# Performance work log

Hardware: AMD Instinct MI355X
Metric: run time of the kernel (lower is better)

Reference implementation:

```python
import jax, jax.numpy as jnp
import numpy as np
import math

IN_SRC, IN_DST, OUT, H = 64, 64, 128, 8
DK = OUT // H


def setup_inputs() -> dict:
    key = jax.random.key(0)
    ks = jax.random.split(key, 24)
    f = lambda k, shp, s=0.05: (jax.random.normal(k, shp, dtype=jnp.float32) * s)
    B, n, m = 16, 256, 128
    inp = {
        'h_dst': jax.random.normal(ks[0], (B, n, IN_DST), dtype=jnp.float32),
        'h_src': jax.random.normal(ks[1], (B, m, IN_SRC), dtype=jnp.float32),
        'h_edge': jax.random.normal(ks[2], (B, n, m), dtype=jnp.float32),
        'ope_ma_adj': jax.random.randint(ks[3], (B, n, m), 0, 2, dtype=jnp.int32),
        'ope_oo_adj': jax.random.randint(ks[4], (B, n, n), 0, 2, dtype=jnp.int32),
        'batch_idxes': jnp.arange(B, dtype=jnp.int64),
        'Wq': f(ks[5], (OUT, IN_DST)), 'bq': f(ks[6], (OUT,)),
        'Wk': f(ks[7], (OUT, IN_SRC)), 'bk': f(ks[8], (OUT,)),
        'Wkd': f(ks[9], (OUT, IN_DST)), 'bkd': f(ks[10], (OUT,)),
        'Wke': f(ks[11], (OUT, 1)), 'bke': f(ks[12], (OUT,)),
        'Wv': f(ks[13], (OUT, IN_SRC)), 'bv': f(ks[14], (OUT,)),
        'Wvd': f(ks[15], (OUT, IN_DST)), 'bvd': f(ks[16], (OUT,)),
        'Wa': f(ks[17], (OUT, OUT)), 'ba': f(ks[18], (OUT,)),
        'rel_pri': jnp.ones((2, H), dtype=jnp.float32),
        'rel_att': f(ks[19], (2, H, DK, DK), 0.2),
        'rel_msg': f(ks[20], (2, H, DK, DK), 0.2),
        'skip': jnp.ones((1,), dtype=jnp.float32),
    }
    return inp


def reference(h_dst, h_src, h_edge, ope_ma_adj, ope_oo_adj, batch_idxes,
              Wq, bq, Wk, bk, Wkd, bkd, Wke, bke, Wv, bv, Wvd, bvd, Wa, ba,
              rel_pri, rel_att, rel_msg, skip):
    B = batch_idxes.shape[0]
    n, m = h_dst.shape[1], h_src.shape[1]
    adj_ma = ope_ma_adj[batch_idxes].astype(jnp.float32)  # [B,n,m]
    adj_oo = ope_oo_adj[batch_idxes].astype(jnp.float32)  # [B,n,n]
    inv_sqrt_dk = 1.0 / math.sqrt(DK)
    # torch einsum 'abcd,abdd->abcd' multiplies by the diagonal of the relation matrix
    dA0 = jnp.diagonal(rel_att[0], axis1=-2, axis2=-1)  # [H,DK]
    dA1 = jnp.diagonal(rel_att[1], axis1=-2, axis2=-1)
    dM0 = jnp.diagonal(rel_msg[0], axis1=-2, axis2=-1)
    dM1 = jnp.diagonal(rel_msg[1], axis1=-2, axis2=-1)

    q = (h_dst @ Wq.T + bq).reshape(B, n, H, DK)           # [B,n,H,DK]
    k = ((h_src @ Wk.T + bk).reshape(B, m, H, DK)) * dA0   # [B,m,H,DK]
    scale0 = rel_pri[0] * inv_sqrt_dk                      # [H]
    m_o_att = jnp.einsum('bnhd,bmhd->bnmh', q, k) * scale0

    # edge projection: Linear(1->OUT) on h_edge[...,None]
    edge = (h_edge[..., None] * Wke[:, 0] + bke).reshape(B, n, m, H, DK) * dA0
    ee = jnp.einsum('bnhd,bnmhd->bnmh', q, edge) * scale0
    m_att = jax.nn.leaky_relu(adj_ma[..., None] * m_o_att + ee, 0.1)

    kd = ((h_dst @ Wkd.T + bkd).reshape(B, n, H, DK)) * dA1
    scale1 = rel_pri[1] * inv_sqrt_dk
    o_att = jax.nn.leaky_relu(adj_oo[..., None] * jnp.einsum('bnhd,bmhd->bnmh', q, kd) * scale1, 0.1)

    att = jnp.concatenate([m_att, o_att], axis=2)          # [B,n,m+n,H]
    mask = jnp.concatenate([adj_ma, adj_oo], axis=2)[..., None] == 1
    att = jax.nn.softmax(jnp.where(mask, att, -1e9), axis=2)
    att_m, att_o = att[:, :, :m], att[:, :, m:]

    v = ((h_src @ Wv.T + bv).reshape(B, m, H, DK)) * dM0   # [B,m,H,DK]
    # m_res_msg = edge + v[:,None]; weighted sum over m (no [B,n,m,H,DK] extra alloc)
    a_m = (jnp.einsum('bnmh,bnmhd->bnhd', att_m, edge)
           + jnp.einsum('bnmh,bmhd->bnhd', att_m, v))
    c = ((h_dst @ Wvd.T + bvd).reshape(B, n, H, DK)) * dM1
    # o_res_msg[b,i,j] = c[b,i] + c[b,j]; weighted sum over j
    a_o = (jnp.einsum('bnjh,bjhd->bnhd', att_o, c)
           + att_o.sum(axis=2)[..., None] * c)

    res = (a_m + a_o).reshape(B, n, OUT)
    trans = jax.nn.gelu(res, approximate=False) @ Wa.T + ba
    alpha = jax.nn.sigmoid(skip[0])
    out = trans * alpha + q.reshape(B, n, OUT) * (1.0 - alpha)
    return out
```

## Files before the change

### kernel.cpp

```cpp
#include <hip/hip_runtime.h>
#include <math.h>

#define H 8
#define DK 16
#define OUTC 128
#define INC 64
#define NB 16
#define NN 256
#define NM 128

typedef float f32x4 __attribute__((ext_vector_type(4)));
typedef short s16x4 __attribute__((ext_vector_type(4)));
typedef short s16x8 __attribute__((ext_vector_type(8)));

#if __has_builtin(__builtin_amdgcn_mfma_f32_16x16x16bf16_1k)
__device__ __forceinline__ f32x4 MFMA16(s16x4 a, s16x4 b, f32x4 c) {
    return __builtin_amdgcn_mfma_f32_16x16x16bf16_1k(a, b, c, 0, 0, 0);
}
#else
__device__ __forceinline__ f32x4 MFMA16(s16x4 a, s16x4 b, f32x4 c) {
    s16x8 a8 = {a[0], a[1], a[2], a[3], 0, 0, 0, 0};
    s16x8 b8 = {b[0], b[1], b[2], b[3], 0, 0, 0, 0};
    return __builtin_amdgcn_mfma_f32_16x16x32_bf16(a8, b8, c, 0, 0, 0);
}
#endif

__device__ __forceinline__ unsigned short f2bf(float x) {
    unsigned int u = __float_as_uint(x);
    return (unsigned short)((u + 0x7fffu + ((u >> 16) & 1u)) >> 16);
}
__device__ __forceinline__ float bf2f(unsigned short s) {
    return __uint_as_float(((unsigned int)s) << 16);
}

__global__ __launch_bounds__(256) void proj_pack(
    const float* __restrict__ h_dst, const float* __restrict__ h_src,
    const int* __restrict__ adj_ma, const int* __restrict__ adj_oo,
    const float* __restrict__ Wq, const float* __restrict__ bq,
    const float* __restrict__ Wk, const float* __restrict__ bk,
    const float* __restrict__ Wkd, const float* __restrict__ bkd,
    const float* __restrict__ Wv, const float* __restrict__ bv,
    const float* __restrict__ Wvd, const float* __restrict__ bvd,
    const float* __restrict__ rel_pri, const float* __restrict__ rel_att,
    const float* __restrict__ rel_msg,
    float* __restrict__ qbuf, unsigned short* __restrict__ qpk,
    unsigned short* __restrict__ kpk, unsigned short* __restrict__ vcb,
    unsigned long long* __restrict__ mk)
{
    __shared__ float X_s[64 * 68];
    __shared__ float WT_s[64 * 128];

    int t = threadIdx.x;
    int bid = blockIdx.x;

    if (bid >= 256) {
        int w = ((bid - 256) << 2) + (t >> 6);
        int l = t & 63;
        #pragma unroll
        for (int i = 0; i < 16; ++i) {
            int flat = w * 16 + i;
            int row = flat / 6, g = flat - row * 6;
            int a = (g < 2) ? adj_ma[(long)row * NM + (g << 6) + l]
                            : adj_oo[(long)row * NN + ((g - 2) << 6) + l];
            unsigned long long m = __ballot(a != 0);
            if (l == 0) mk[flat] = m;
        }
        return;
    }

    int type, grow0;
    const float *X, *W, *bias;
    if (bid < 64)        { type = 0; grow0 = bid * 64;        X = h_dst; W = Wq;  bias = bq;  }
    else if (bid < 128)  { type = 2; grow0 = (bid-64) * 64;   X = h_dst; W = Wkd; bias = bkd; }
    else if (bid < 192)  { type = 4; grow0 = (bid-128) * 64;  X = h_dst; W = Wvd; bias = bvd; }
    else if (bid < 224)  { type = 1; grow0 = (bid-192) * 64;  X = h_src; W = Wk;  bias = bk;  }
    else                 { type = 3; grow0 = (bid-224) * 64;  X = h_src; W = Wv;  bias = bv;  }

    #pragma unroll
    for (int p = 0; p < 4; ++p) {
        int idx = t + 256 * p;
        int row = idx >> 4, part = idx & 15;
        float4 v = *(const float4*)(X + (long)(grow0 + row) * INC + part * 4);
        *(float4*)(X_s + row * 68 + part * 4) = v;
    }
    #pragma unroll
    for (int p = 0; p < 8; ++p) {
        int idx = t + 256 * p;
        int o = idx >> 4, part = idx & 15;
        float4 v = *(const float4*)(W + (long)o * INC + part * 4);
        int q0 = o >> 2, ob = o & 3;
        WT_s[(part*4+0)*128 + (((q0 ^ ((part*4+0)&31))<<2) + ob)] = v.x;
        WT_s[(part*4+1)*128 + (((q0 ^ ((part*4+1)&31))<<2) + ob)] = v.y;
        WT_s[(part*4+2)*128 + (((q0 ^ ((part*4+2)&31))<<2) + ob)] = v.z;
        WT_s[(part*4+3)*128 + (((q0 ^ ((part*4+3)&31))<<2) + ob)] = v.w;
    }
    __syncthreads();

    int o4 = t & 31;
    int rq = t >> 5;
    float4 acc[8];
    #pragma unroll
    for (int rr = 0; rr < 8; ++rr) acc[rr] = make_float4(0.f, 0.f, 0.f, 0.f);

    #pragma unroll 4
    for (int i4 = 0; i4 < 16; ++i4) {
        float4 w0 = *(const float4*)(WT_s + (i4*4+0)*128 + ((o4 ^ ((i4*4+0)&31))<<2));
        float4 w1 = *(const float4*)(WT_s + (i4*4+1)*128 + ((o4 ^ ((i4*4+1)&31))<<2));
        float4 w2 = *(const float4*)(WT_s + (i4*4+2)*128 + ((o4 ^ ((i4*4+2)&31))<<2));
        float4 w3 = *(const float4*)(WT_s + (i4*4+3)*128 + ((o4 ^ ((i4*4+3)&31))<<2));
        #pragma unroll
        for (int rr = 0; rr < 8; ++rr) {
            float4 x = *(const float4*)(X_s + (rq + 8*rr) * 68 + i4*4);
            acc[rr].x += x.x*w0.x + x.y*w1.x + x.z*w2.x + x.w*w3.x;
            acc[rr].y += x.x*w0.y + x.y*w1.y + x.z*w2.y + x.w*w3.y;
            acc[rr].z += x.x*w0.z + x.y*w1.z + x.z*w2.z + x.w*w3.z;
            acc[rr].w += x.x*w0.w + x.y*w1.w + x.z*w2.w + x.w*w3.w;
        }
    }

    int obase = o4 * 4;
    int head = o4 >> 2;
    float4 bs = *(const float4*)(bias + obase);
    float scl[4];
    #pragma unroll
    for (int c = 0; c < 4; ++c) {
        int o = obase + c;
        int hh = o >> 4, d = o & 15;
        float v = 1.f;
        if (type == 1)      v = rel_pri[hh]     * 0.25f * rel_att[(hh*DK + d)*DK + d];
        else if (type == 2) v = rel_pri[H + hh] * 0.25f * rel_att[((H + hh)*DK + d)*DK + d];
        else if (type == 3) v = rel_msg[(hh*DK + d)*DK + d];
        else if (type == 4) v = rel_msg[((H + hh)*DK + d)*DK + d];
        scl[c] = v;
    }
    #pragma unroll
    for (int rr = 0; rr < 8; ++rr) {
        int grow = grow0 + rq + 8*rr;
        float4 r4;
        r4.x = (acc[rr].x + bs.x) * scl[0];
        r4.y = (acc[rr].y + bs.y) * scl[1];
        r4.z = (acc[rr].z + bs.z) * scl[2];
        r4.w = (acc[rr].w + bs.w) * scl[3];
        unsigned int lo = (unsigned int)f2bf(r4.x) | ((unsigned int)f2bf(r4.y) << 16);
        unsigned int hi = (unsigned int)f2bf(r4.z) | ((unsigned int)f2bf(r4.w) << 16);
        uint2 pk = make_uint2(lo, hi);
        if (type == 0) {
            *(float4*)(qbuf + (long)grow * OUTC + obase) = r4;
            int b = grow >> 8, row = grow & 255;
            int lane = ((o4 & 3) << 4) + (row & 15);
            ((uint2*)qpk)[(long)((b*H + head)*16 + (row >> 4)) * 64 + lane] = pk;
        } else if (type == 1 || type == 2) {
            int b, key;
            if (type == 1) { b = grow >> 7; key = grow & 127; }
            else           { b = grow >> 8; key = 128 + (grow & 255); }
            int lane = (key & 15) + ((o4 & 3) << 4);
            ((uint2*)kpk)[(long)((b*H + head)*24 + (key >> 4)) * 64 + lane] = pk;
        } else {
            int b, key;
            if (type == 3) { b = grow >> 7; key = grow & 127; }
            else           { b = grow >> 8; key = 128 + (grow & 255); }
            ((uint2*)vcb)[(long)((b*H + head)*384 + key) * 4 + (o4 & 3)] = pk;
        }
    }
}

__global__ __launch_bounds__(256) void hgt_main5(
    const float* __restrict__ h_edge,
    const unsigned long long* __restrict__ mkbuf,
    const float* __restrict__ Wke, const float* __restrict__ bke,
    const float* __restrict__ rel_pri, const float* __restrict__ rel_att,
    const float* __restrict__ qbuf,
    const unsigned short* __restrict__ qpk,
    const unsigned short* __restrict__ kpk,
    const unsigned short* __restrict__ vcb,
    float* __restrict__ gelbuf)
{
    __shared__ unsigned short kpk_s[6144];
    __shared__ unsigned short vpk_s[6144];
    __shared__ float he_s[128 * 65];
    __shared__ unsigned long long mk_s[384];
    __shared__ float stats_s[256];
    __shared__ float s1s2_s[128];

    int t = threadIdx.x;
    int bid = blockIdx.x;
    int qb = bid & 3;
    int bh = bid >> 2;
    int h = bh & 7;
    int b = bh >> 3;
    int row0 = b * NN + qb * 64;

    {
        const uint4* src = (const uint4*)(kpk + (long)bh * 6144);
        uint4* dst = (uint4*)kpk_s;
        #pragma unroll
        for (int p = 0; p < 3; ++p) dst[t + 256*p] = src[t + 256*p];
    }
    #pragma unroll
    for (int p = 0; p < 6; ++p) {
        int idx = t + 256 * p;
        int key = idx >> 2, dc = idx & 3;
        uint2 v = ((const uint2*)(vcb + (long)bh * 6144))[key * 4 + dc];
        int base = (key >> 4) * 256 + ((((key >> 2) & 3) << 4) + dc * 4) * 4 + (key & 3);
        vpk_s[base     ] = (unsigned short)(v.x & 0xffffu);
        vpk_s[base + 4 ] = (unsigned short)(v.x >> 16);
        vpk_s[base + 8 ] = (unsigned short)(v.y & 0xffffu);
        vpk_s[base + 12] = (unsigned short)(v.y >> 16);
    }
    #pragma unroll
    for (int p = 0; p < 8; ++p) {
        int idx = t + 256 * p;
        int q = idx >> 5, jc = (idx & 31) << 2;
        float4 v = *(const float4*)(h_edge + (long)(row0 + q) * NM + jc);
        he_s[(jc+0)*65 + q] = v.x;
        he_s[(jc+1)*65 + q] = v.y;
        he_s[(jc+2)*65 + q] = v.z;
        he_s[(jc+3)*65 + q] = v.w;
    }
    for (int i = t; i < 384; i += 256) mk_s[i] = mkbuf[(long)row0 * 6 + i];
    if (t < 64) {
        const float* qr = qbuf + (long)(row0 + t) * OUTC + h * DK;
        float s1 = 0.f, s2 = 0.f;
        #pragma unroll
        for (int d = 0; d < DK; ++d) {
            int o = h * DK + d;
            float qq = qr[d] * rel_att[o * DK + d];
            s1 += qq * Wke[o];
            s2 += qq * bke[o];
        }
        float sc = rel_pri[h] * 0.25f;
        s1s2_s[t*2]   = s1 * sc;
        s1s2_s[t*2+1] = s2 * sc;
    }
    __syncthreads();

    int w = t >> 6, l = t & 63;
    int qi = l & 15;
    int grpb = (l >> 4) << 2;
    int qloc = w * 16 + qi;

    union { uint2 u; s16x4 s; } qf;
    qf.u = ((const uint2*)qpk)[(long)(bh * 16 + qb * 4 + w) * 64 + l];

    float S1q = s1s2_s[qloc * 2], S2q = s1s2_s[qloc * 2 + 1];
    unsigned int mdw[12];
    #pragma unroll
    for (int i = 0; i < 12; ++i) mdw[i] = ((const unsigned int*)(mk_s + qloc * 6))[i];

    float sum = 0.f, t0 = 0.f, t1 = 0.f, so = 0.f;
    f32x4 O0 = {0.f, 0.f, 0.f, 0.f};
    f32x4 O1 = {0.f, 0.f, 0.f, 0.f};
    const f32x4 zero = {0.f, 0.f, 0.f, 0.f};

    #pragma unroll
    for (int tt = 0; tt < 24; ++tt) {
        s16x4 kf = *(const s16x4*)(kpk_s + tt * 256 + l * 4);
        f32x4 s4 = MFMA16(kf, qf.s, zero);

        unsigned int dw = mdw[tt >> 1];
        int sb = ((tt & 1) << 4) + grpb;
        float ev[4], hev[4];
        #pragma unroll
        for (int r = 0; r < 4; ++r) {
            float x = s4[r];
            if (tt < 8) {
                hev[r] = he_s[(tt * 16 + grpb + r) * 65 + qloc];
                x += hev[r] * S1q + S2q;
            }
            float lk = fmaxf(x, 0.1f * x);
            float ex = __expf(lk);
            ev[r] = ((dw >> (sb + r)) & 1u) ? ex : 0.f;
        }
        float es = (ev[0] + ev[1]) + (ev[2] + ev[3]);
        sum += es;
        if (tt < 8) {
            t0 += es;
            t1 += (ev[0]*hev[0] + ev[1]*hev[1]) + (ev[2]*hev[2] + ev[3]*hev[3]);
        } else {
            so += es;
        }
        s16x4 p;
        p[0] = (short)f2bf(ev[0]); p[1] = (short)f2bf(ev[1]);
        p[2] = (short)f2bf(ev[2]); p[3] = (short)f2bf(ev[3]);
        s16x4 vf = *(const s16x4*)(vpk_s + tt * 256 + l * 4);
        if (tt & 1) O1 = MFMA16(p, vf, O1);
        else        O0 = MFMA16(p, vf, O0);
    }
    f32x4 O = O0 + O1;

    sum += __shfl_xor(sum, 16); sum += __shfl_xor(sum, 32);
    t0  += __shfl_xor(t0, 16);  t0  += __shfl_xor(t0, 32);
    t1  += __shfl_xor(t1, 16);  t1  += __shfl_xor(t1, 32);
    so  += __shfl_xor(so, 16);  so  += __shfl_xor(so, 32);
    if (l < 16) {
        float4 st = make_float4(1.f / sum, t0, t1, so);
        *(float4*)(stats_s + (w * 16 + l) * 4) = st;
    }

    int d = qi;
    int o = h * DK + d;
    float a0 = rel_att[o * DK + d];
    float wk = Wke[o], bk = bke[o];
    #pragma unroll
    for (int r = 0; r < 4; ++r) {
        int ql = w * 16 + grpb + r;
        float4 st = *(const float4*)(stats_s + ql * 4);
        int key = 128 + qb * 64 + ql;
        float cs = bf2f(vpk_s[(key >> 4) * 256 + ((((key >> 2) & 3) << 4) + d) * 4 + (key & 3)]);
        float res = st.x * (O[r] + a0 * (wk * st.z + bk * st.y) + st.w * cs);
        float g = 0.5f * res * (1.f + erff(res * 0.70710678118654752f));
        gelbuf[(long)(row0 + ql) * OUTC + o] = g;
    }
}

__global__ __launch_bounds__(256) void out_gemm(
    const float* __restrict__ gelbuf, const float* __restrict__ qbuf,
    const float* __restrict__ Wa, const float* __restrict__ ba,
    const float* __restrict__ skip, float* __restrict__ outp)
{
    __shared__ float WaT[128 * 128];
    __shared__ float gel_s[16 * 132];

    int t = threadIdx.x;
    long row0 = (long)blockIdx.x * 16;

    #pragma unroll
    for (int p = 0; p < 16; ++p) {
        int idx = t + 256 * p;
        int o = idx >> 5, part = idx & 31;
        float4 v = *(const float4*)(Wa + (long)o * OUTC + part * 4);
        int q0 = o >> 2, ob = o & 3;
        WaT[(part*4+0)*128 + (((q0 ^ ((part*4+0)&31))<<2) + ob)] = v.x;
        WaT[(part*4+1)*128 + (((q0 ^ ((part*4+1)&31))<<2) + ob)] = v.y;
        WaT[(part*4+2)*128 + (((q0 ^ ((part*4+2)&31))<<2) + ob)] = v.z;
        WaT[(part*4+3)*128 + (((q0 ^ ((part*4+3)&31))<<2) + ob)] = v.w;
    }
    #pragma unroll
    for (int p = 0; p < 2; ++p) {
        int idx = t + 256 * p;
        int row = idx >> 5, part = idx & 31;
        float4 v = *(const float4*)(gelbuf + (row0 + row) * OUTC + part * 4);
        *(float4*)(gel_s + row * 132 + part * 4) = v;
    }
    __syncthreads();

    int o4 = t & 31, rp = t >> 5;
    float4 acc0 = make_float4(0.f,0.f,0.f,0.f);
    float4 acc1 = make_float4(0.f,0.f,0.f,0.f);
    #pragma unroll 4
    for (int i4 = 0; i4 < 32; ++i4) {
        float4 w0 = *(const float4*)(WaT + (i4*4+0)*128 + ((o4 ^ ((i4*4+0)&31))<<2));
        float4 w1 = *(const float4*)(WaT + (i4*4+1)*128 + ((o4 ^ ((i4*4+1)&31))<<2));
        float4 w2 = *(const float4*)(WaT + (i4*4+2)*128 + ((o4 ^ ((i4*4+2)&31))<<2));
        float4 w3 = *(const float4*)(WaT + (i4*4+3)*128 + ((o4 ^ ((i4*4+3)&31))<<2));
        float4 x0 = *(const float4*)(gel_s + rp * 132 + i4*4);
        float4 x1 = *(const float4*)(gel_s + (rp+8) * 132 + i4*4);
        acc0.x += x0.x*w0.x + x0.y*w1.x + x0.z*w2.x + x0.w*w3.x;
        acc0.y += x0.x*w0.y + x0.y*w1.y + x0.z*w2.y + x0.w*w3.y;
        acc0.z += x0.x*w0.z + x0.y*w1.z + x0.z*w2.z + x0.w*w3.z;
        acc0.w += x0.x*w0.w + x0.y*w1.w + x0.z*w2.w + x0.w*w3.w;
        acc1.x += x1.x*w0.x + x1.y*w1.x + x1.z*w2.x + x1.w*w3.x;
        acc1.y += x1.x*w0.y + x1.y*w1.y + x1.z*w2.y + x1.w*w3.y;
        acc1.z += x1.x*w0.z + x1.y*w1.z + x1.z*w2.z + x1.w*w3.z;
        acc1.w += x1.x*w0.w + x1.y*w1.w + x1.z*w2.w + x1.w*w3.w;
    }

    float alpha = 1.f / (1.f + __expf(-skip[0]));
    float beta = 1.f - alpha;
    float4 bs = *(const float4*)(ba + o4*4);
    {
        float4 q0 = *(const float4*)(qbuf + (row0 + rp) * OUTC + o4*4);
        float4 r0;
        r0.x = alpha*(acc0.x + bs.x) + beta*q0.x;
        r0.y = alpha*(acc0.y + bs.y) + beta*q0.y;
        r0.z = alpha*(acc0.z + bs.z) + beta*q0.z;
        r0.w = alpha*(acc0.w + bs.w) + beta*q0.w;
        *(float4*)(outp + (row0 + rp) * OUTC + o4*4) = r0;
    }
    {
        float4 q1 = *(const float4*)(qbuf + (row0 + rp + 8) * OUTC + o4*4);
        float4 r1;
        r1.x = alpha*(acc1.x + bs.x) + beta*q1.x;
        r1.y = alpha*(acc1.y + bs.y) + beta*q1.y;
        r1.z = alpha*(acc1.z + bs.z) + beta*q1.z;
        r1.w = alpha*(acc1.w + bs.w) + beta*q1.w;
        *(float4*)(outp + (row0 + rp + 8) * OUTC + o4*4) = r1;
    }
}

extern "C" void kernel_launch(void* const* d_in, const int* in_sizes, int n_in,
                              void* d_out, int out_size, void* d_ws, size_t ws_size,
                              hipStream_t stream) {
    const float* h_dst  = (const float*)d_in[0];
    const float* h_src  = (const float*)d_in[1];
    const float* h_edge = (const float*)d_in[2];
    const int*   adj_ma = (const int*)d_in[3];
    const int*   adj_oo = (const int*)d_in[4];
    const float* Wq  = (const float*)d_in[6];
    const float* bq  = (const float*)d_in[7];
    const float* Wk  = (const float*)d_in[8];
    const float* bk  = (const float*)d_in[9];
    const float* Wkd = (const float*)d_in[10];
    const float* bkd = (const float*)d_in[11];
    const float* Wke = (const float*)d_in[12];
    const float* bke = (const float*)d_in[13];
    const float* Wv  = (const float*)d_in[14];
    const float* bv  = (const float*)d_in[15];
    const float* Wvd = (const float*)d_in[16];
    const float* bvd = (const float*)d_in[17];
    const float* Wa  = (const float*)d_in[18];
    const float* ba  = (const float*)d_in[19];
    const float* rel_pri = (const float*)d_in[20];
    const float* rel_att = (const float*)d_in[21];
    const float* rel_msg = (const float*)d_in[22];
    const float* skip    = (const float*)d_in[23];

    char* ws = (char*)d_ws;
    float* qbuf   = (float*)ws;
    float* gelbuf = (float*)(ws + 2097152);
    unsigned short* kpk = (unsigned short*)(ws + 4194304);
    unsigned short* qpk = (unsigned short*)(ws + 5767168);
    unsigned short* vcb = (unsigned short*)(ws + 6815744);
    unsigned long long* mkbuf = (unsigned long long*)(ws + 8388608);

    proj_pack<<<640, 256, 0, stream>>>(h_dst, h_src, adj_ma, adj_oo,
                                       Wq, bq, Wk, bk, Wkd, bkd, Wv, bv, Wvd, bvd,
                                       rel_pri, rel_att, rel_msg,
                                       qbuf, qpk, kpk, vcb, mkbuf);

    hgt_main5<<<NB * H * 4, 256, 0, stream>>>(
        h_edge, mkbuf, Wke, bke, rel_pri, rel_att,
        qbuf, qpk, kpk, vcb, gelbuf);

    out_gemm<<<NB * NN / 16, 256, 0, stream>>>(gelbuf, qbuf, Wa, ba, skip, (float*)d_out);
}
```

Baseline: 39.16 us.

## Fuse three kernels into one cooperative persistent kernel with grid syncs

After: 127.6 us. +225.7%, slower.

```diff
diff --git a/kernel.cpp b/kernel.cpp
--- a/kernel.cpp
+++ b/kernel.cpp
@@ -1,5 +1,8 @@
 #include <hip/hip_runtime.h>
+#include <hip/hip_cooperative_groups.h>
 #include <math.h>
+
+namespace cg = cooperative_groups;
 
 #define H 8
 #define DK 16
@@ -33,48 +36,44 @@
     return __uint_as_float(((unsigned int)s) << 16);
 }
 
-__global__ __launch_bounds__(256) void proj_pack(
-    const float* __restrict__ h_dst, const float* __restrict__ h_src,
-    const int* __restrict__ adj_ma, const int* __restrict__ adj_oo,
-    const float* __restrict__ Wq, const float* __restrict__ bq,
-    const float* __restrict__ Wk, const float* __restrict__ bk,
-    const float* __restrict__ Wkd, const float* __restrict__ bkd,
-    const float* __restrict__ Wv, const float* __restrict__ bv,
-    const float* __restrict__ Wvd, const float* __restrict__ bvd,
-    const float* __restrict__ rel_pri, const float* __restrict__ rel_att,
-    const float* __restrict__ rel_msg,
-    float* __restrict__ qbuf, unsigned short* __restrict__ qpk,
-    unsigned short* __restrict__ kpk, unsigned short* __restrict__ vcb,
-    unsigned long long* __restrict__ mk)
-{
-    __shared__ float X_s[64 * 68];
-    __shared__ float WT_s[64 * 128];
-
-    int t = threadIdx.x;
-    int bid = blockIdx.x;
-
-    if (bid >= 256) {
-        int w = ((bid - 256) << 2) + (t >> 6);
+struct KArgs {
+    const float* h_dst; const float* h_src; const float* h_edge;
+    const int* adj_ma; const int* adj_oo;
+    const float* Wq; const float* bq; const float* Wk; const float* bk;
+    const float* Wkd; const float* bkd; const float* Wke; const float* bke;
+    const float* Wv; const float* bv; const float* Wvd; const float* bvd;
+    const float* Wa; const float* ba;
+    const float* rel_pri; const float* rel_att; const float* rel_msg;
+    const float* skip;
+    float* qbuf; unsigned short* qpk; unsigned short* kpk; unsigned short* vcb;
+    unsigned long long* mk; float* gelbuf; float* outp;
+};
+
+__device__ __forceinline__ void proj_unit_body(const KArgs& A, int unit, int t,
+                                               float* X_s, float* WT_s)
+{
+    if (unit >= 256) {
+        int w = ((unit - 256) << 2) + (t >> 6);
         int l = t & 63;
         #pragma unroll
         for (int i = 0; i < 16; ++i) {
             int flat = w * 16 + i;
             int row = flat / 6, g = flat - row * 6;
-            int a = (g < 2) ? adj_ma[(long)row * NM + (g << 6) + l]
-                            : adj_oo[(long)row * NN + ((g - 2) << 6) + l];
+            int a = (g < 2) ? A.adj_ma[(long)row * NM + (g << 6) + l]
+                            : A.adj_oo[(long)row * NN + ((g - 2) << 6) + l];
             unsigned long long m = __ballot(a != 0);
-            if (l == 0) mk[flat] = m;
+            if (l == 0) A.mk[flat] = m;
         }
         return;
     }
 
     int type, grow0;
     const float *X, *W, *bias;
-    if (bid < 64)        { type = 0; grow0 = bid * 64;        X = h_dst; W = Wq;  bias = bq;  }
-    else if (bid < 128)  { type = 2; grow0 = (bid-64) * 64;   X = h_dst; W = Wkd; bias = bkd; }
-    else if (bid < 192)  { type = 4; grow0 = (bid-128) * 64;  X = h_dst; W = Wvd; bias = bvd; }
-    else if (bid < 224)  { type = 1; grow0 = (bid-192) * 64;  X = h_src; W = Wk;  bias = bk;  }
-    else                 { type = 3; grow0 = (bid-224) * 64;  X = h_src; W = Wv;  bias = bv;  }
+    if (unit < 64)        { type = 0; grow0 = unit * 64;        X = A.h_dst; W = A.Wq;  bias = A.bq;  }
+    else if (unit < 128)  { type = 2; grow0 = (unit-64) * 64;   X = A.h_dst; W = A.Wkd; bias = A.bkd; }
+    else if (unit < 192)  { type = 4; grow0 = (unit-128) * 64;  X = A.h_dst; W = A.Wvd; bias = A.bvd; }
+    else if (unit < 224)  { type = 1; grow0 = (unit-192) * 64;  X = A.h_src; W = A.Wk;  bias = A.bk;  }
+    else                  { type = 3; grow0 = (unit-224) * 64;  X = A.h_src; W = A.Wv;  bias = A.bv;  }
 
     #pragma unroll
     for (int p = 0; p < 4; ++p) {
@@ -127,10 +126,10 @@
         int o = obase + c;
         int hh = o >> 4, d = o & 15;
         float v = 1.f;
-        if (type == 1)      v = rel_pri[hh]     * 0.25f * rel_att[(hh*DK + d)*DK + d];
-        else if (type == 2) v = rel_pri[H + hh] * 0.25f * rel_att[((H + hh)*DK + d)*DK + d];
-        else if (type == 3) v = rel_msg[(hh*DK + d)*DK + d];
-        else if (type == 4) v = rel_msg[((H + hh)*DK + d)*DK + d];
+        if (type == 1)      v = A.rel_pri[hh]     * 0.25f * A.rel_att[(hh*DK + d)*DK + d];
+        else if (type == 2) v = A.rel_pri[H + hh] * 0.25f * A.rel_att[((H + hh)*DK + d)*DK + d];
+        else if (type == 3) v = A.rel_msg[(hh*DK + d)*DK + d];
+        else if (type == 4) v = A.rel_msg[((H + hh)*DK + d)*DK + d];
         scl[c] = v;
     }
     #pragma unroll
@@ -145,53 +144,37 @@
         unsigned int hi = (unsigned int)f2bf(r4.z) | ((unsigned int)f2bf(r4.w) << 16);
         uint2 pk = make_uint2(lo, hi);
         if (type == 0) {
-            *(float4*)(qbuf + (long)grow * OUTC + obase) = r4;
+            *(float4*)(A.qbuf + (long)grow * OUTC + obase) = r4;
             int b = grow >> 8, row = grow & 255;
             int lane = ((o4 & 3) << 4) + (row & 15);
-            ((uint2*)qpk)[(long)((b*H + head)*16 + (row >> 4)) * 64 + lane] = pk;
+            ((uint2*)A.qpk)[(long)((b*H + head)*16 + (row >> 4)) * 64 + lane] = pk;
         } else if (type == 1 || type == 2) {
             int b, key;
             if (type == 1) { b = grow >> 7; key = grow & 127; }
             else           { b = grow >> 8; key = 128 + (grow & 255); }
             int lane = (key & 15) + ((o4 & 3) << 4);
-            ((uint2*)kpk)[(long)((b*H + head)*24 + (key >> 4)) * 64 + lane] = pk;
+            ((uint2*)A.kpk)[(long)((b*H + head)*24 + (key >> 4)) * 64 + lane] = pk;
         } else {
             int b, key;
             if (type == 3) { b = grow >> 7; key = grow & 127; }
             else           { b = grow >> 8; key = 128 + (grow & 255); }
-            ((uint2*)vcb)[(long)((b*H + head)*384 + key) * 4 + (o4 & 3)] = pk;
-        }
-    }
-}
-
-__global__ __launch_bounds__(256) void hgt_main5(
-    const float* __restrict__ h_edge,
-    const unsigned long long* __restrict__ mkbuf,
-    const float* __restrict__ Wke, const float* __restrict__ bke,
-    const float* __restrict__ rel_pri, const float* __restrict__ rel_att,
-    const float* __restrict__ qbuf,
-    const unsigned short* __restrict__ qpk,
-    const unsigned short* __restrict__ kpk,
-    const unsigned short* __restrict__ vcb,
-    float* __restrict__ gelbuf)
-{
-    __shared__ unsigned short kpk_s[6144];
-    __shared__ unsigned short vpk_s[6144];
-    __shared__ float he_s[128 * 65];
-    __shared__ unsigned long long mk_s[384];
-    __shared__ float stats_s[256];
-    __shared__ float s1s2_s[128];
-
-    int t = threadIdx.x;
-    int bid = blockIdx.x;
-    int qb = bid & 3;
-    int bh = bid >> 2;
+            ((uint2*)A.vcb)[(long)((b*H + head)*384 + key) * 4 + (o4 & 3)] = pk;
+        }
+    }
+}
+
+__device__ __forceinline__ void attn_unit_body(const KArgs& A, int unit, int t,
+    unsigned short* kpk_s, unsigned short* vpk_s, float* he_s,
+    unsigned long long* mk_s, float* stats_s, float* s1s2_s)
+{
+    int qb = unit & 3;
+    int bh = unit >> 2;
     int h = bh & 7;
     int b = bh >> 3;
     int row0 = b * NN + qb * 64;
 
     {
-        const uint4* src = (const uint4*)(kpk + (long)bh * 6144);
+        const uint4* src = (const uint4*)(A.kpk + (long)bh * 6144);
         uint4* dst = (uint4*)kpk_s;
         #pragma unroll
         for (int p = 0; p < 3; ++p) dst[t + 256*p] = src[t + 256*p];
@@ -200,7 +183,7 @@
     for (int p = 0; p < 6; ++p) {
         int idx = t + 256 * p;
         int key = idx >> 2, dc = idx & 3;
-        uint2 v = ((const uint2*)(vcb + (long)bh * 6144))[key * 4 + dc];
+        uint2 v = ((const uint2*)(A.vcb + (long)bh * 6144))[key * 4 + dc];
         int base = (key >> 4) * 256 + ((((key >> 2) & 3) << 4) + dc * 4) * 4 + (key & 3);
         vpk_s[base     ] = (unsigned short)(v.x & 0xffffu);
         vpk_s[base + 4 ] = (unsigned short)(v.x >> 16);
@@ -211,24 +194,24 @@
     for (int p = 0; p < 8; ++p) {
         int idx = t + 256 * p;
         int q = idx >> 5, jc = (idx & 31) << 2;
-        float4 v = *(const float4*)(h_edge + (long)(row0 + q) * NM + jc);
+        float4 v = *(const float4*)(A.h_edge + (long)(row0 + q) * NM + jc);
         he_s[(jc+0)*65 + q] = v.x;
         he_s[(jc+1)*65 + q] = v.y;
         he_s[(jc+2)*65 + q] = v.z;
         he_s[(jc+3)*65 + q] = v.w;
     }
-    for (int i = t; i < 384; i += 256) mk_s[i] = mkbuf[(long)row0 * 6 + i];
+    for (int i = t; i < 384; i += 256) mk_s[i] = A.mk[(long)row0 * 6 + i];
     if (t < 64) {
-        const float* qr = qbuf + (long)(row0 + t) * OUTC + h * DK;
+        const float* qr = A.qbuf + (long)(row0 + t) * OUTC + h * DK;
         float s1 = 0.f, s2 = 0.f;
         #pragma unroll
         for (int d = 0; d < DK; ++d) {
             int o = h * DK + d;
-            float qq = qr[d] * rel_att[o * DK + d];
-            s1 += qq * Wke[o];
-            s2 += qq * bke[o];
-        }
-        float sc = rel_pri[h] * 0.25f;
+            float qq = qr[d] * A.rel_att[o * DK + d];
+            s1 += qq * A.Wke[o];
+            s2 += qq * A.bke[o];
+        }
+        float sc = A.rel_pri[h] * 0.25f;
         s1s2_s[t*2]   = s1 * sc;
         s1s2_s[t*2+1] = s2 * sc;
     }
@@ -240,7 +223,7 @@
     int qloc = w * 16 + qi;
 
     union { uint2 u; s16x4 s; } qf;
-    qf.u = ((const uint2*)qpk)[(long)(bh * 16 + qb * 4 + w) * 64 + l];
+    qf.u = ((const uint2*)A.qpk)[(long)(bh * 16 + qb * 4 + w) * 64 + l];
 
     float S1q = s1s2_s[qloc * 2], S2q = s1s2_s[qloc * 2 + 1];
     unsigned int mdw[12];
@@ -299,8 +282,8 @@
 
     int d = qi;
     int o = h * DK + d;
-    float a0 = rel_att[o * DK + d];
-    float wk = Wke[o], bk = bke[o];
+    float a0 = A.rel_att[o * DK + d];
+    float wk = A.Wke[o], bk = A.bke[o];
     #pragma unroll
     for (int r = 0; r < 4; ++r) {
         int ql = w * 16 + grpb + r;
@@ -309,128 +292,169 @@
         float cs = bf2f(vpk_s[(key >> 4) * 256 + ((((key >> 2) & 3) << 4) + d) * 4 + (key & 3)]);
         float res = st.x * (O[r] + a0 * (wk * st.z + bk * st.y) + st.w * cs);
         float g = 0.5f * res * (1.f + erff(res * 0.70710678118654752f));
-        gelbuf[(long)(row0 + ql) * OUTC + o] = g;
-    }
-}
-
-__global__ __launch_bounds__(256) void out_gemm(
-    const float* __restrict__ gelbuf, const float* __restrict__ qbuf,
-    const float* __restrict__ Wa, const float* __restrict__ ba,
-    const float* __restrict__ skip, float* __restrict__ outp)
-{
-    __shared__ float WaT[128 * 128];
-    __shared__ float gel_s[16 * 132];
-
-    int t = threadIdx.x;
-    long row0 = (long)blockIdx.x * 16;
-
-    #pragma unroll
-    for (int p = 0; p < 16; ++p) {
-        int idx = t + 256 * p;
-        int o = idx >> 5, part = idx & 31;
-        float4 v = *(const float4*)(Wa + (long)o * OUTC + part * 4);
-        int q0 = o >> 2, ob = o & 3;
-        WaT[(part*4+0)*128 + (((q0 ^ ((part*4+0)&31))<<2) + ob)] = v.x;
-        WaT[(part*4+1)*128 + (((q0 ^ ((part*4+1)&31))<<2) + ob)] = v.y;
-        WaT[(part*4+2)*128 + (((q0 ^ ((part*4+2)&31))<<2) + ob)] = v.z;
-        WaT[(part*4+3)*128 + (((q0 ^ ((part*4+3)&31))<<2) + ob)] = v.w;
-    }
+        A.gelbuf[(long)(row0 + ql) * OUTC + o] = g;
+    }
+}
+
+__device__ __forceinline__ void out_unit_body(const KArgs& A, int unit, int t,
+                                              float* gel_s, float* WT_s)
+{
+    long row0 = (long)unit * 16;
+
     #pragma unroll
     for (int p = 0; p < 2; ++p) {
         int idx = t + 256 * p;
         int row = idx >> 5, part = idx & 31;
-        float4 v = *(const float4*)(gelbuf + (row0 + row) * OUTC + part * 4);
+        float4 v = *(const float4*)(A.gelbuf + (row0 + row) * OUTC + part * 4);
         *(float4*)(gel_s + row * 132 + part * 4) = v;
     }
-    __syncthreads();
-
-    int o4 = t & 31, rp = t >> 5;
-    float4 acc0 = make_float4(0.f,0.f,0.f,0.f);
-    float4 acc1 = make_float4(0.f,0.f,0.f,0.f);
-    #pragma unroll 4
-    for (int i4 = 0; i4 < 32; ++i4) {
-        float4 w0 = *(const float4*)(WaT + (i4*4+0)*128 + ((o4 ^ ((i4*4+0)&31))<<2));
-        float4 w1 = *(const float4*)(WaT + (i4*4+1)*128 + ((o4 ^ ((i4*4+1)&31))<<2));
-        float4 w2 = *(const float4*)(WaT + (i4*4+2)*128 + ((o4 ^ ((i4*4+2)&31))<<2));
-        float4 w3 = *(const float4*)(WaT + (i4*4+3)*128 + ((o4 ^ ((i4*4+3)&31))<<2));
-        float4 x0 = *(const float4*)(gel_s + rp * 132 + i4*4);
-        float4 x1 = *(const float4*)(gel_s + (rp+8) * 132 + i4*4);
-        acc0.x += x0.x*w0.x + x0.y*w1.x + x0.z*w2.x + x0.w*w3.x;
-        acc0.y += x0.x*w0.y + x0.y*w1.y + x0.z*w2.y + x0.w*w3.y;
-        acc0.z += x0.x*w0.z + x0.y*w1.z + x0.z*w2.z + x0.w*w3.z;
-        acc0.w += x0.x*w0.w + x0.y*w1.w + x0.z*w2.w + x0.w*w3.w;
-        acc1.x += x1.x*w0.x + x1.y*w1.x + x1.z*w2.x + x1.w*w3.x;
-        acc1.y += x1.x*w0.y + x1.y*w1.y + x1.z*w2.y + x1.w*w3.y;
-        acc1.z += x1.x*w0.z + x1.y*w1.z + x1.z*w2.z + x1.w*w3.z;
-        acc1.w += x1.x*w0.w + x1.y*w1.w + x1.z*w2.w + x1.w*w3.w;
-    }
-
-    float alpha = 1.f / (1.f + __expf(-skip[0]));
+
+    float alpha = 1.f / (1.f + __expf(-A.skip[0]));
     float beta = 1.f - alpha;
-    float4 bs = *(const float4*)(ba + o4*4);
+
+    #pragma unroll
+    for (int pass = 0; pass < 2; ++pass) {
+        __syncthreads();
+        #pragma unroll
+        for (int p = 0; p < 8; ++p) {
+            int idx = t + 256 * p;
+            int ol = idx >> 5, part = idx & 31;
+            float4 v = *(const float4*)(A.Wa + (long)(pass*64 + ol) * OUTC + part * 4);
+            WT_s[(part*4+0)*68 + ol] = v.x;
+            WT_s[(part*4+1)*68 + ol] = v.y;
+            WT_s[(part*4+2)*68 + ol] = v.z;
+            WT_s[(part*4+3)*68 + ol] = v.w;
+        }
+        __syncthreads();
+
+        int o4 = t & 15, rp = t >> 4;
+        float4 acc = make_float4(0.f,0.f,0.f,0.f);
+        #pragma unroll 4
+        for (int i4 = 0; i4 < 32; ++i4) {
+            float4 w0 = *(const float4*)(WT_s + (i4*4+0)*68 + o4*4);
+            float4 w1 = *(const float4*)(WT_s + (i4*4+1)*68 + o4*4);
+            float4 w2 = *(const float4*)(WT_s + (i4*4+2)*68 + o4*4);
+            float4 w3 = *(const float4*)(WT_s + (i4*4+3)*68 + o4*4);
+            float4 x0 = *(const float4*)(gel_s + rp * 132 + i4*4);
+            acc.x += x0.x*w0.x + x0.y*w1.x + x0.z*w2.x + x0.w*w3.x;
+            acc.y += x0.x*w0.y + x0.y*w1.y + x0.z*w2.y + x0.w*w3.y;
+            acc.z += x0.x*w0.z + x0.y*w1.z + x0.z*w2.z + x0.w*w3.z;
+            acc.w += x0.x*w0.w + x0.y*w1.w + x0.z*w2.w + x0.w*w3.w;
+        }
+
+        int obase = pass*64 + o4*4;
+        float4 bs = *(const float4*)(A.ba + obase);
+        float4 q0 = *(const float4*)(A.qbuf + (row0 + rp) * OUTC + obase);
+        float4 r0;
+        r0.x = alpha*(acc.x + bs.x) + beta*q0.x;
+        r0.y = alpha*(acc.y + bs.y) + beta*q0.y;
+        r0.z = alpha*(acc.z + bs.z) + beta*q0.z;
+        r0.w = alpha*(acc.w + bs.w) + beta*q0.w;
+        *(float4*)(A.outp + (row0 + rp) * OUTC + obase) = r0;
+    }
+}
+
+__global__ __launch_bounds__(256, 2) void hgt_fused(KArgs A)
+{
+    __shared__ __align__(16) unsigned char smem[62464];
+    int t = threadIdx.x;
+    cg::grid_group grid = cg::this_grid();
+
+    for (int unit = blockIdx.x; unit < 640; unit += 256) {
+        proj_unit_body(A, unit, t, (float*)smem, (float*)(smem + 17408));
+        __syncthreads();
+    }
+
+    grid.sync();
+
     {
-        float4 q0 = *(const float4*)(qbuf + (row0 + rp) * OUTC + o4*4);
-        float4 r0;
-        r0.x = alpha*(acc0.x + bs.x) + beta*q0.x;
-        r0.y = alpha*(acc0.y + bs.y) + beta*q0.y;
-        r0.z = alpha*(acc0.z + bs.z) + beta*q0.z;
-        r0.w = alpha*(acc0.w + bs.w) + beta*q0.w;
-        *(float4*)(outp + (row0 + rp) * OUTC + o4*4) = r0;
-    }
-    {
-        float4 q1 = *(const float4*)(qbuf + (row0 + rp + 8) * OUTC + o4*4);
-        float4 r1;
-        r1.x = alpha*(acc1.x + bs.x) + beta*q1.x;
-        r1.y = alpha*(acc1.y + bs.y) + beta*q1.y;
-        r1.z = alpha*(acc1.z + bs.z) + beta*q1.z;
-        r1.w = alpha*(acc1.w + bs.w) + beta*q1.w;
-        *(float4*)(outp + (row0 + rp + 8) * OUTC + o4*4) = r1;
-    }
+        unsigned short* kpk_s = (unsigned short*)smem;
+        unsigned short* vpk_s = (unsigned short*)(smem + 12288);
+        float* he_s = (float*)(smem + 24576);
+        unsigned long long* mk_s = (unsigned long long*)(smem + 57856);
+        float* stats_s = (float*)(smem + 60928);
+        float* s1s2_s  = (float*)(smem + 61952);
+        #pragma unroll
+        for (int it = 0; it < 2; ++it) {
+            attn_unit_body(A, blockIdx.x + 256 * it, t,
+                           kpk_s, vpk_s, he_s, mk_s, stats_s, s1s2_s);
+            __syncthreads();
+        }
+    }
+
+    grid.sync();
+
+    out_unit_body(A, blockIdx.x, t, (float*)smem, (float*)(smem + 8448));
+}
+
+__global__ __launch_bounds__(256) void proj_pack_k(KArgs A)
+{
+    __shared__ __align__(16) unsigned char smem[50176];
+    proj_unit_body(A, blockIdx.x, threadIdx.x, (float*)smem, (float*)(smem + 17408));
+}
+
+__global__ __launch_bounds__(256) void hgt_main_k(KArgs A)
+{
+    __shared__ __align__(16) unsigned char smem[62464];
+    unsigned short* kpk_s = (unsigned short*)smem;
+    unsigned short* vpk_s = (unsigned short*)(smem + 12288);
+    float* he_s = (float*)(smem + 24576);
+    unsigned long long* mk_s = (unsigned long long*)(smem + 57856);
+    float* stats_s = (float*)(smem + 60928);
+    float* s1s2_s  = (float*)(smem + 61952);
+    attn_unit_body(A, blockIdx.x, threadIdx.x, kpk_s, vpk_s, he_s, mk_s, stats_s, s1s2_s);
+}
+
+__global__ __launch_bounds__(256) void out_gemm_k(KArgs A)
+{
+    __shared__ __align__(16) unsigned char smem[43264];
+    out_unit_body(A, blockIdx.x, threadIdx.x, (float*)smem, (float*)(smem + 8448));
 }
 
 extern "C" void kernel_launch(void* const* d_in, const int* in_sizes, int n_in,
                               void* d_out, int out_size, void* d_ws, size_t ws_size,
                               hipStream_t stream) {
-    const float* h_dst  = (const float*)d_in[0];
-    const float* h_src  = (const float*)d_in[1];
-    const float* h_edge = (const float*)d_in[2];
-    const int*   adj_ma = (const int*)d_in[3];
-    const int*   adj_oo = (const int*)d_in[4];
-    const float* Wq  = (const float*)d_in[6];
-    const float* bq  = (const float*)d_in[7];
-    const float* Wk  = (const float*)d_in[8];
-    const float* bk  = (const float*)d_in[9];
-    const float* Wkd = (const float*)d_in[10];
-    const float* bkd = (const float*)d_in[11];
-    const float* Wke = (const float*)d_in[12];
-    const float* bke = (const float*)d_in[13];
-    const float* Wv  = (const float*)d_in[14];
-    const float* bv  = (const float*)d_in[15];
-    const float* Wvd = (const float*)d_in[16];
-    const float* bvd = (const float*)d_in[17];
-    const float* Wa  = (const float*)d_in[18];
-    const float* ba  = (const float*)d_in[19];
-    const float* rel_pri = (const float*)d_in[20];
-    const float* rel_att = (const float*)d_in[21];
-    const float* rel_msg = (const float*)d_in[22];
-    const float* skip    = (const float*)d_in[23];
-
     char* ws = (char*)d_ws;
-    float* qbuf   = (float*)ws;
-    float* gelbuf = (float*)(ws + 2097152);
-    unsigned short* kpk = (unsigned short*)(ws + 4194304);
-    unsigned short* qpk = (unsigned short*)(ws + 5767168);
-    unsigned short* vcb = (unsigned short*)(ws + 6815744);
-    unsigned long long* mkbuf = (unsigned long long*)(ws + 8388608);
-
-    proj_pack<<<640, 256, 0, stream>>>(h_dst, h_src, adj_ma, adj_oo,
-                                       Wq, bq, Wk, bk, Wkd, bkd, Wv, bv, Wvd, bvd,
-                                       rel_pri, rel_att, rel_msg,
-                                       qbuf, qpk, kpk, vcb, mkbuf);
-
-    hgt_main5<<<NB * H * 4, 256, 0, stream>>>(
-        h_edge, mkbuf, Wke, bke, rel_pri, rel_att,
-        qbuf, qpk, kpk, vcb, gelbuf);
-
-    out_gemm<<<NB * NN / 16, 256, 0, stream>>>(gelbuf, qbuf, Wa, ba, skip, (float*)d_out);
-}
+    KArgs A;
+    A.h_dst  = (const float*)d_in[0];
+    A.h_src  = (const float*)d_in[1];
+    A.h_edge = (const float*)d_in[2];
+    A.adj_ma = (const int*)d_in[3];
+    A.adj_oo = (const int*)d_in[4];
+    A.Wq  = (const float*)d_in[6];
+    A.bq  = (const float*)d_in[7];
+    A.Wk  = (const float*)d_in[8];
+    A.bk  = (const float*)d_in[9];
+    A.Wkd = (const float*)d_in[10];
+    A.bkd = (const float*)d_in[11];
+    A.Wke = (const float*)d_in[12];
+    A.bke = (const float*)d_in[13];
+    A.Wv  = (const float*)d_in[14];
+    A.bv  = (const float*)d_in[15];
+    A.Wvd = (const float*)d_in[16];
+    A.bvd = (const float*)d_in[17];
+    A.Wa  = (const float*)d_in[18];
+    A.ba  = (const float*)d_in[19];
+    A.rel_pri = (const float*)d_in[20];
+    A.rel_att = (const float*)d_in[21];
+    A.rel_msg = (const float*)d_in[22];
+    A.skip    = (const float*)d_in[23];
+
+    A.qbuf   = (float*)ws;
+    A.gelbuf = (float*)(ws + 2097152);
+    A.kpk = (unsigned short*)(ws + 4194304);
+    A.qpk = (unsigned short*)(ws + 5767168);
+    A.vcb = (unsigned short*)(ws + 6815744);
+    A.mk  = (unsigned long long*)(ws + 8388608);
+    A.outp = (float*)d_out;
+
+    void* kargs[] = { (void*)&A };
+    hipError_t err = hipLaunchCooperativeKernel((const void*)hgt_fused,
+                                                dim3(256), dim3(256),
+                                                kargs, 0, stream);
+    if (err != hipSuccess) {
+        proj_pack_k<<<640, 256, 0, stream>>>(A);
+        hgt_main_k<<<512, 256, 0, stream>>>(A);
+        out_gemm_k<<<256, 256, 0, stream>>>(A);
+    }
+}
```
